# Kernel optimization log

Hardware: AMD Instinct MI355X
Metric: run time of the kernel (lower is better)

Reference implementation:

```python
import jax, jax.numpy as jnp
import numpy as np

TEMPERATURE = 0.5
B, D = 4096, 256


def setup_inputs() -> dict:
    key = jax.random.key(0)
    k1, k2 = jax.random.split(key)
    emb_i = jax.random.normal(k1, (B, D), dtype=jnp.float32)
    emb_j = jax.random.normal(k2, (B, D), dtype=jnp.float32)
    return {"emb_i": emb_i, "emb_j": emb_j}


def reference(emb_i, emb_j):
    # NT-Xent (SimCLR) loss, vectorized version of the per-sample python loop.
    n = emb_i.shape[0]
    eps = 1e-12
    z_i = emb_i / jnp.maximum(jnp.linalg.norm(emb_i, axis=1, keepdims=True), eps)
    z_j = emb_j / jnp.maximum(jnp.linalg.norm(emb_j, axis=1, keepdims=True), eps)
    reps = jnp.concatenate([z_i, z_j], axis=0)               # [2N, D], unit rows
    # cosine similarity of unit vectors == dot product
    sim = reps @ reps.T                                       # [2N, 2N]
    exp_sim = jnp.exp(sim / TEMPERATURE)
    # denominator for row i: sum over k != i of exp(sim[i,k]/T)
    denom = jnp.sum(exp_sim, axis=1) - jnp.diagonal(exp_sim)  # [2N]
    # positive-pair sims: sim[k, k+N] and sim[k+N, k]
    pos = jnp.concatenate([jnp.diagonal(sim[:n, n:]), jnp.diagonal(sim[n:, :n])])
    # l_ij = log(exp(pos/T) / denom) = pos/T - log(denom)
    loss_terms = pos / TEMPERATURE - jnp.log(denom)
    return (1.0 / (2 * n)) * jnp.sum(loss_terms)
```

## Files before the change

kernel.cpp:

```cpp
#include <hip/hip_runtime.h>
#include <math.h>


#define NROWS 8192
#define NHALF 4096
#define DIM   256
#define BM    128
#define BN    128
#define NCB   (NROWS / BN)
#define NTRI  (NCB * (NCB + 1) / 2)

typedef __attribute__((ext_vector_type(8))) short bf16x8;
typedef __attribute__((ext_vector_type(4))) float f32x4;

static __device__ __forceinline__ unsigned short f2bf(float x) {
  unsigned int u = __float_as_uint(x);
  unsigned int r = (u + 0x7FFFu + ((u >> 16) & 1u)) >> 16;
  return (unsigned short)r;
}

__global__ __launch_bounds__(256) void normalize_kernel(
    const float* __restrict__ emb_i, const float* __restrict__ emb_j,
    unsigned short* __restrict__ zbF, float* __restrict__ out) {
  __shared__ unsigned short tile[16 * DIM];
  if (blockIdx.x == 0 && threadIdx.x == 0) out[0] = 0.f;
  const int w = threadIdx.x >> 6, lane = threadIdx.x & 63;
  const int rg = blockIdx.x;
  #pragma unroll
  for (int rr = 0; rr < 4; ++rr) {
    const int m16 = w * 4 + rr;
    const int row = rg * 16 + m16;
    const float* src = (row < NHALF) ? (emb_i + (size_t)row * DIM)
                                     : (emb_j + (size_t)(row - NHALF) * DIM);
    float4 v = ((const float4*)src)[lane];
    float ss = v.x * v.x + v.y * v.y + v.z * v.z + v.w * v.w;
    #pragma unroll
    for (int off = 32; off; off >>= 1) ss += __shfl_down(ss, off, 64);
    float total = __shfl(ss, 0, 64);
    float inv = 1.41421356237f / fmaxf(sqrtf(total), 1e-12f);
    ushort4 o;
    o.x = f2bf(v.x * inv); o.y = f2bf(v.y * inv);
    o.z = f2bf(v.z * inv); o.w = f2bf(v.w * inv);
    const int ks = lane >> 3, quad = (lane >> 1) & 3, jj = (lane & 1) * 4;
    *(ushort4*)&tile[ks * 512 + (quad * 16 + m16) * 8 + jj] = o;
  }
  __syncthreads();
  uint4* dst = (uint4*)(zbF + (size_t)rg * (16 * DIM));
  const uint4* srcT = (const uint4*)tile;
  dst[threadIdx.x] = srcT[threadIdx.x];
  dst[256 + threadIdx.x] = srcT[256 + threadIdx.x];
}

__global__ __launch_bounds__(256, 3) void denom_kernel(
    const unsigned short* __restrict__ zbF, float* __restrict__ denomP,
    float* __restrict__ posv) {
  __shared__ float red[512];

  int t = blockIdx.x;
  int by = (int)((sqrtf(8.0f * (float)t + 1.0f) - 1.0f) * 0.5f);
  while ((by + 1) * (by + 2) / 2 <= t) ++by;
  while (by * (by + 1) / 2 > t) --by;
  int bx = t - by * (by + 1) / 2;

  const int tid = threadIdx.x;
  const int w = tid >> 6;
  const int lane = tid & 63;
  const int wr = w >> 1, wc = w & 1;
  const int quad = lane >> 4;
  const int m16 = lane & 15;
  const int row0 = bx * BM;
  const int col0 = by * BN;

  const unsigned short* pA[4];
  const unsigned short* pB[4];
  #pragma unroll
  for (int i = 0; i < 4; ++i) {
    pA[i] = zbF + (size_t)(bx * 8 + wr * 4 + i) * 4096 + lane * 8;
    pB[i] = zbF + (size_t)(by * 8 + wc * 4 + i) * 4096 + lane * 8;
  }

  f32x4 acc[4][4];
  #pragma unroll
  for (int i = 0; i < 4; ++i)
    #pragma unroll
    for (int j = 0; j < 4; ++j) {
      f32x4 z4 = {0.f, 0.f, 0.f, 0.f};
      acc[i][j] = z4;
    }

#define LOADAB(A, B, ks)                                          \
  do {                                                            \
    _Pragma("unroll") for (int i = 0; i < 4; ++i) {               \
      A[i] = *(const bf16x8*)(pA[i] + (ks) * 512);                \
      B[i] = *(const bf16x8*)(pB[i] + (ks) * 512);                \
    }                                                             \
  } while (0)

#define MFMA16(A, B)                                              \
  do {                                                            \
    _Pragma("unroll") for (int i = 0; i < 4; ++i)                 \
        _Pragma("unroll") for (int j = 0; j < 4; ++j)             \
            acc[i][j] = __builtin_amdgcn_mfma_f32_16x16x32_bf16(  \
                A[i], B[j], acc[i][j], 0, 0, 0);                  \
  } while (0)

  bf16x8 aE[4], bE[4], aO[4], bO[4];
  LOADAB(aE, bE, 0);
  LOADAB(aO, bO, 1);
  #pragma unroll
  for (int k2 = 0; k2 < 4; ++k2) {
    MFMA16(aE, bE);
    if (k2 < 3) LOADAB(aE, bE, 2 * k2 + 2);
    MFMA16(aO, bO);
    if (k2 < 3) LOADAB(aO, bO, 2 * k2 + 3);
  }
#undef LOADAB
#undef MFMA16

  if (col0 - row0 == NHALF) {
    #pragma unroll
    for (int i = 0; i < 4; ++i)
      #pragma unroll
      for (int j = 0; j < 4; ++j) {
        int gcol = col0 + wc * 64 + j * 16 + m16;
        #pragma unroll
        for (int r = 0; r < 4; ++r) {
          int grow = row0 + wr * 64 + i * 16 + quad * 4 + r;
          if (gcol - grow == NHALF) posv[grow] = acc[i][j][r];
        }
      }
  }

  float rs[4][4];
  float cs[4] = {0.f, 0.f, 0.f, 0.f};
  #pragma unroll
  for (int i = 0; i < 4; ++i)
    #pragma unroll
    for (int r = 0; r < 4; ++r) rs[i][r] = 0.f;

  if (bx != by) {
    #pragma unroll
    for (int i = 0; i < 4; ++i)
      #pragma unroll
      for (int j = 0; j < 4; ++j)
        #pragma unroll
        for (int r = 0; r < 4; ++r) {
          float e = __expf(acc[i][j][r]);
          rs[i][r] += e;
          cs[j] += e;
        }
  } else {
    #pragma unroll
    for (int i = 0; i < 4; ++i)
      #pragma unroll
      for (int j = 0; j < 4; ++j) {
        int gcol = col0 + wc * 64 + j * 16 + m16;
        #pragma unroll
        for (int r = 0; r < 4; ++r) {
          int grow = row0 + wr * 64 + i * 16 + quad * 4 + r;
          float e = (grow == gcol) ? 0.f : __expf(acc[i][j][r]);
          rs[i][r] += e;
          cs[j] += e;
        }
      }
  }

  #pragma unroll
  for (int i = 0; i < 4; ++i)
    #pragma unroll
    for (int r = 0; r < 4; ++r) {
      float v = rs[i][r];
      v += __shfl_xor(v, 1, 16);
      v += __shfl_xor(v, 2, 16);
      v += __shfl_xor(v, 4, 16);
      v += __shfl_xor(v, 8, 16);
      if (m16 == 0) red[wc * 128 + wr * 64 + i * 16 + quad * 4 + r] = v;
    }
  #pragma unroll
  for (int j = 0; j < 4; ++j) {
    float v = cs[j];
    v += __shfl_xor(v, 16, 64);
    v += __shfl_xor(v, 32, 64);
    if (quad == 0) red[256 + wr * 128 + wc * 64 + j * 16 + m16] = v;
  }
  __syncthreads();

  if (tid < 128) {
    denomP[(size_t)by * NROWS + row0 + tid] = red[tid] + red[128 + tid];
  } else if (bx != by) {
    int c = tid - 128;
    denomP[(size_t)bx * NROWS + col0 + c] = red[256 + c] + red[384 + c];
  }
}

__global__ __launch_bounds__(256) void reduce_kernel(
    const float* __restrict__ denomP, const float* __restrict__ posv,
    float* __restrict__ out) {
  int tid = threadIdx.x;
  int r = blockIdx.x * 256 + tid;
  float s = 0.f;
  #pragma unroll 8
  for (int b = 0; b < NCB; ++b) s += denomP[(size_t)b * NROWS + r];
  float v = -logf(s);
  if (r < NHALF) v += 2.0f * posv[r];
  #pragma unroll
  for (int off = 32; off; off >>= 1) v += __shfl_down(v, off, 64);
  __shared__ float s4[4];
  if ((tid & 63) == 0) s4[tid >> 6] = v;
  __syncthreads();
  if (tid == 0)
    atomicAdd(out, (s4[0] + s4[1] + s4[2] + s4[3]) * (1.0f / 8192.0f));
}

extern "C" void kernel_launch(void* const* d_in, const int* in_sizes, int n_in,
                              void* d_out, int out_size, void* d_ws,
                              size_t ws_size, hipStream_t stream) {
  const float* emb_i = (const float*)d_in[0];
  const float* emb_j = (const float*)d_in[1];
  unsigned short* zbF = (unsigned short*)d_ws;
  float* denomP = (float*)(zbF + (size_t)NROWS * DIM);
  float* posv = denomP + (size_t)NCB * NROWS;
  float* out = (float*)d_out;

  normalize_kernel<<<NROWS / 16, 256, 0, stream>>>(emb_i, emb_j, zbF, out);
  denom_kernel<<<NTRI, 256, 0, stream>>>(zbF, denomP, posv);
  reduce_kernel<<<NROWS / 256, 256, 0, stream>>>(denomP, posv, out);
}
```

Baseline: 99.85 us.

## Stage A tile in LDS via direct global-to-LDS loads and use native exp2

The row tile (A) of each triangular block is now loaded once into shared memory with global_load_lds and read from LDS by the four waves, instead of each wave re-reading it from global memory. The normalization scale is folded to sqrt(2/ln2) so the exponent can use the hardware exp2 instruction directly, with the positive-pair coefficient adjusted to match. MFMA phases are wrapped with s_setprio to favor matrix issue. The 64 KB LDS buffer lowers occupancy, and launch bounds drop from 3 to 2 blocks per CU.

```diff
diff --git a/kernel.cpp b/kernel.cpp
--- a/kernel.cpp
+++ b/kernel.cpp
@@ -37,7 +37,7 @@
     #pragma unroll
     for (int off = 32; off; off >>= 1) ss += __shfl_down(ss, off, 64);
     float total = __shfl(ss, 0, 64);
-    float inv = 1.41421356237f / fmaxf(sqrtf(total), 1e-12f);
+    float inv = 1.69870011f / fmaxf(sqrtf(total), 1e-12f);
     ushort4 o;
     o.x = f2bf(v.x * inv); o.y = f2bf(v.y * inv);
     o.z = f2bf(v.z * inv); o.w = f2bf(v.w * inv);
@@ -51,9 +51,10 @@
   dst[256 + threadIdx.x] = srcT[256 + threadIdx.x];
 }
 
-__global__ __launch_bounds__(256, 3) void denom_kernel(
+__global__ __launch_bounds__(256, 2) void denom_kernel(
     const unsigned short* __restrict__ zbF, float* __restrict__ denomP,
     float* __restrict__ posv) {
+  __shared__ unsigned short As[64 * 512];
   __shared__ float red[512];
 
   int t = blockIdx.x;
@@ -71,13 +72,23 @@
   const int row0 = bx * BM;
   const int col0 = by * BN;
 
-  const unsigned short* pA[4];
+  {
+    const unsigned short* zbA = zbF + (size_t)(bx * 8) * 4096 + lane * 8;
+    #pragma unroll
+    for (int tt = 0; tt < 16; ++tt) {
+      const int chunk = w * 16 + tt;
+      __builtin_amdgcn_global_load_lds(
+          (const __attribute__((address_space(1))) unsigned int*)(zbA +
+                                                                  chunk * 512),
+          (__attribute__((address_space(3))) unsigned int*)&As[chunk * 512],
+          16, 0, 0);
+    }
+  }
+
   const unsigned short* pB[4];
   #pragma unroll
-  for (int i = 0; i < 4; ++i) {
-    pA[i] = zbF + (size_t)(bx * 8 + wr * 4 + i) * 4096 + lane * 8;
-    pB[i] = zbF + (size_t)(by * 8 + wc * 4 + i) * 4096 + lane * 8;
-  }
+  for (int j = 0; j < 4; ++j)
+    pB[j] = zbF + (size_t)(by * 8 + wc * 4 + j) * 4096 + lane * 8;
 
   f32x4 acc[4][4];
   #pragma unroll
@@ -88,33 +99,50 @@
       acc[i][j] = z4;
     }
 
-#define LOADAB(A, B, ks)                                          \
-  do {                                                            \
-    _Pragma("unroll") for (int i = 0; i < 4; ++i) {               \
-      A[i] = *(const bf16x8*)(pA[i] + (ks) * 512);                \
-      B[i] = *(const bf16x8*)(pB[i] + (ks) * 512);                \
-    }                                                             \
+#define LOADA(A, ks)                                                       \
+  do {                                                                     \
+    _Pragma("unroll") for (int i = 0; i < 4; ++i)                          \
+        A[i] = *(const bf16x8*)&As[((wr * 4 + i) * 8 + (ks)) * 512 +       \
+                                   lane * 8];                              \
   } while (0)
 
-#define MFMA16(A, B)                                              \
-  do {                                                            \
-    _Pragma("unroll") for (int i = 0; i < 4; ++i)                 \
-        _Pragma("unroll") for (int j = 0; j < 4; ++j)             \
-            acc[i][j] = __builtin_amdgcn_mfma_f32_16x16x32_bf16(  \
-                A[i], B[j], acc[i][j], 0, 0, 0);                  \
+#define LOADB(B, ks)                                                       \
+  do {                                                                     \
+    _Pragma("unroll") for (int j = 0; j < 4; ++j)                          \
+        B[j] = *(const bf16x8*)(pB[j] + (ks) * 512);                       \
   } while (0)
 
+#define MFMA16(A, B)                                                       \
+  do {                                                                     \
+    __builtin_amdgcn_s_setprio(1);                                         \
+    _Pragma("unroll") for (int i = 0; i < 4; ++i)                          \
+        _Pragma("unroll") for (int j = 0; j < 4; ++j)                      \
+            acc[i][j] = __builtin_amdgcn_mfma_f32_16x16x32_bf16(           \
+                A[i], B[j], acc[i][j], 0, 0, 0);                           \
+    __builtin_amdgcn_s_setprio(0);                                         \
+  } while (0)
+
   bf16x8 aE[4], bE[4], aO[4], bO[4];
-  LOADAB(aE, bE, 0);
-  LOADAB(aO, bO, 1);
+  LOADB(bE, 0);
+  LOADB(bO, 1);
+  __syncthreads();
+  LOADA(aE, 0);
+  LOADA(aO, 1);
   #pragma unroll
   for (int k2 = 0; k2 < 4; ++k2) {
     MFMA16(aE, bE);
-    if (k2 < 3) LOADAB(aE, bE, 2 * k2 + 2);
+    if (k2 < 3) {
+      LOADB(bE, 2 * k2 + 2);
+      LOADA(aE, 2 * k2 + 2);
+    }
     MFMA16(aO, bO);
-    if (k2 < 3) LOADAB(aO, bO, 2 * k2 + 3);
-  }
-#undef LOADAB
+    if (k2 < 3) {
+      LOADB(bO, 2 * k2 + 3);
+      LOADA(aO, 2 * k2 + 3);
+    }
+  }
+#undef LOADA
+#undef LOADB
 #undef MFMA16
 
   if (col0 - row0 == NHALF) {
@@ -145,7 +173,7 @@
       for (int j = 0; j < 4; ++j)
         #pragma unroll
         for (int r = 0; r < 4; ++r) {
-          float e = __expf(acc[i][j][r]);
+          float e = __builtin_amdgcn_exp2f(acc[i][j][r]);
           rs[i][r] += e;
           cs[j] += e;
         }
@@ -158,7 +186,8 @@
         #pragma unroll
         for (int r = 0; r < 4; ++r) {
           int grow = row0 + wr * 64 + i * 16 + quad * 4 + r;
-          float e = (grow == gcol) ? 0.f : __expf(acc[i][j][r]);
+          float e =
+              (grow == gcol) ? 0.f : __builtin_amdgcn_exp2f(acc[i][j][r]);
           rs[i][r] += e;
           cs[j] += e;
         }
@@ -202,7 +231,7 @@
   #pragma unroll 8
   for (int b = 0; b < NCB; ++b) s += denomP[(size_t)b * NROWS + r];
   float v = -logf(s);
-  if (r < NHALF) v += 2.0f * posv[r];
+  if (r < NHALF) v += 1.38629436112f * posv[r];
   #pragma unroll
   for (int off = 32; off; off >>= 1) v += __shfl_down(v, off, 64);
   __shared__ float s4[4];
```

Result: no change. 99.27 us (-0.6%).
